# Kernel tuning notes

Hardware: AMD Instinct MI355X
Metric: run time of the kernel (lower is better)

The kernel has to match this reference:

```python
import math
import jax, jax.numpy as jnp
import numpy as np

COULOMB = 14.399645478425668  # eV*Angstrom / e^2


def setup_inputs() -> dict:
    key = jax.random.key(0)
    k0, k1, k2, k3, k4 = jax.random.split(key, 5)
    B, n, F, S = 128, 512, 64, 4  # molecules, atoms/molecule, feat dim, n species
    N = B * n
    node_features = jax.random.normal(k0, (N, F), dtype=jnp.float32)
    pos = jax.random.normal(k1, (N, 3), dtype=jnp.float32) * 5.0  # spread atoms out
    atom_type = jax.random.randint(k2, (N,), 0, S)
    total_charge = jnp.zeros((B, 1), dtype=jnp.float32)
    chi_weight = jax.random.normal(k3, (F, 1), dtype=jnp.float32) / np.float32(np.sqrt(F))
    hardness_param = jnp.ones((S,), dtype=jnp.float32)
    sigma = 0.3 + 0.5 * jax.random.uniform(k4, (S,), dtype=jnp.float32)  # covalent radii
    return dict(node_features=node_features, pos=pos, atom_type=atom_type,
                total_charge=total_charge, chi_weight=chi_weight,
                hardness_param=hardness_param, sigma=sigma, n_per_mol=n)


def reference(node_features, pos, atom_type, total_charge, chi_weight,
              hardness_param, sigma, n_per_mol):
    n = n_per_mol
    N, F = node_features.shape
    B = N // n

    feats = node_features.reshape(B, n, F)
    pos_b = pos.reshape(B, n, 3)
    sp = atom_type.reshape(B, n)

    chi = (feats @ chi_weight)[..., 0]                      # [B, n] electronegativity
    hard = jnp.square(hardness_param)[sp]                   # [B, n]
    sig = sigma[sp]                                         # [B, n]

    # pairwise distances within each molecule (diag masked for safe divide)
    diff = pos_b[:, :, None, :] - pos_b[:, None, :, :]      # [B, n, n, 3]
    d2 = jnp.sum(diff * diff, axis=-1)
    eye = jnp.eye(n, dtype=pos.dtype)
    d = jnp.sqrt(jnp.where(eye, 1.0, d2))                   # [B, n, n]

    gamma = jnp.sqrt(sig[:, :, None] ** 2 + sig[:, None, :] ** 2)
    off = COULOMB * jax.lax.erf(d / (math.sqrt(2.0) * gamma)) / d
    diag = hard + COULOMB / (math.sqrt(math.pi) * sig)      # [B, n]
    coeffs = off * (1.0 - eye) + eye * diag[:, :, None]     # [B, n, n]

    # augmented Qeq system with charge-conservation Lagrange multiplier
    A = jnp.ones((B, n + 1, n + 1), dtype=coeffs.dtype)
    A = A.at[:, :n, :n].set(coeffs)
    A = A.at[:, n, n].set(0.0)
    rhs = jnp.concatenate([-chi, total_charge], axis=1)     # [B, n+1]
    sol = jnp.linalg.solve(A, rhs[..., None])[..., 0]
    q = sol[:, :n]                                          # [B, n] charges

    # E = sum_{i<j} C_ij q_i q_j + sum_i (chi_i q_i + 0.5 diag_i q_i^2)
    #   = 0.5 q^T C q + chi . q   (C includes diagonal)
    e_qeq = 0.5 * jnp.einsum('bi,bij,bj->b', q, coeffs, q) + jnp.sum(chi * q, axis=1)
    return e_qeq[:, None], q.reshape(N, 1)
```

## Files before the change

kernel.cpp:

```cpp
#include <hip/hip_runtime.h>
#include <math.h>

#define NA 512
#define NN (NA*NA)
#define COULOMB 14.399645478425668f
#define SQRT_PI 1.7724538509055160273f

__device__ __forceinline__ float rl(float x, int lane) {
    return __int_as_float(__builtin_amdgcn_readlane(__float_as_int(x), lane));
}

__device__ __forceinline__ float pair_val(float dx, float dy, float dz,
                                          float s2i, float s2k) {
    float d2 = dx*dx + dy*dy + dz*dz;
    float rinv = rsqrtf(d2);
    return COULOMB * erff(d2 * rinv * rsqrtf(2.f * (s2i + s2k))) * rinv;
}

__global__ void k_pre(const float* __restrict__ feats, const float* __restrict__ w,
                      const int* __restrict__ type, const float* __restrict__ hard,
                      const float* __restrict__ sigma,
                      float* __restrict__ chi, float* __restrict__ diag,
                      float* __restrict__ sigA, int N) {
    __shared__ float wl[64];
    int tid = threadIdx.x;
    if (tid < 64) wl[tid] = w[tid];
    __syncthreads();
    int i = blockIdx.x * 256 + tid;
    if (i >= N) return;
    const float4* fp = (const float4*)(feats + (size_t)i * 64);
    float acc = 0.f;
#pragma unroll
    for (int q = 0; q < 16; q++) {
        float4 v = fp[q];
        acc += v.x * wl[4*q] + v.y * wl[4*q+1] + v.z * wl[4*q+2] + v.w * wl[4*q+3];
    }
    chi[i] = acc;
    int t = type[i];
    float s = sigma[t];
    float h = hard[t];
    sigA[i] = s;
    diag[i] = h * h + COULOMB / (SQRT_PI * s);
}

__global__ void __launch_bounds__(256, 1) k_panel(const float* __restrict__ pos,
                                                  const float* __restrict__ sigA,
                                                  const float* __restrict__ diagA,
                                                  float* __restrict__ C, const int j) {
    const int q = blockIdx.x;
    const int b = blockIdx.y;
    float* __restrict__ Cb = C + (size_t)b * NN;
    const int jb = j * 64;
    const int m = NA - jb - 64;
    const int tid = threadIdx.x;
    __shared__ float D[64 * 65];
    __shared__ float DT[64 * 64];
    __shared__ float invd[64];
    __shared__ float px[NA], py[NA], pz[NA], s2s[NA];

    if (j == 0) {
#pragma unroll
        for (int e = 0; e < 2; e++) {
            int i = e * 256 + tid;
            px[i] = pos[((size_t)b * NA + i) * 3 + 0];
            py[i] = pos[((size_t)b * NA + i) * 3 + 1];
            pz[i] = pos[((size_t)b * NA + i) * 3 + 2];
            float s = sigA[b * NA + i];
            s2s[i] = s * s;
        }
        __syncthreads();
    }

#pragma unroll
    for (int e = 0; e < 16; e++) {
        int f = e * 256 + tid;
        int rr = f >> 6, cc = f & 63;
        float v;
        if (j == 0) {
            if (rr == cc) v = diagA[b * NA + rr];
            else v = pair_val(px[rr]-px[cc], py[rr]-py[cc], pz[rr]-pz[cc], s2s[rr], s2s[cc]);
        } else {
            v = Cb[(size_t)(jb + rr) * NA + jb + cc];
        }
        D[rr * 65 + cc] = v;
    }

    const int h = m >> 1;
    const int r0 = q ? h : 0;
    const int nr = q ? (m - h) : h;
    const int r = tid - 32;
    const bool hasrow = (r >= 0 && r < nr);
    const int grow = jb + 64 + r0 + r;
    float rv[64];
    if (hasrow) {
        if (j == 0) {
#pragma unroll
            for (int k = 0; k < 64; k++)
                rv[k] = pair_val(px[grow]-px[k], py[grow]-py[k], pz[grow]-pz[k],
                                 s2s[grow], s2s[k]);
        } else {
            const float4* rp = (const float4*)(Cb + (size_t)grow * NA + jb);
#pragma unroll
            for (int qq = 0; qq < 16; qq++) {
                float4 v = rp[qq];
                rv[4*qq] = v.x; rv[4*qq+1] = v.y; rv[4*qq+2] = v.z; rv[4*qq+3] = v.w;
            }
        }
    }
    __syncthreads();

    if (tid < 64) {
        const int t = tid;
        float cl[64];
#pragma unroll
        for (int i = 0; i < 64; i++) cl[i] = (i >= t) ? D[i * 65 + t] : D[t * 65 + i];
#pragma unroll
        for (int k = 0; k < 64; k++) {
            float pivot = rl(cl[k], k);
            float invp = 1.0f / pivot;
            float factor = (t > k) ? (cl[k] * invp) : 0.0f;
#pragma unroll
            for (int i = k + 1; i < 64; i++) {
                float bc = rl(cl[i], k);
                cl[i] -= bc * factor;
            }
        }
        float rs = 1.0f / sqrtf(cl[t]);
        invd[t] = rs;
#pragma unroll
        for (int i = 0; i < 64; i++)
            if (i >= t) D[i * 65 + t] = cl[i] * rs;
    }
    __syncthreads();

#pragma unroll
    for (int e = 0; e < 16; e++) {
        int f = e * 256 + tid;
        int row = f >> 6, cc = f & 63;
        float v = D[row * 65 + cc];
        DT[row * 64 + cc] = (cc < row) ? v : 0.f;
        if (q == 0 && cc <= row) Cb[(size_t)(jb + row) * NA + jb + cc] = v;
    }
    __syncthreads();

    if (hasrow) {
#pragma unroll
        for (int k = 0; k < 64; k++) {
            float acc = rv[k];
            const float4* Lr = (const float4*)(DT + k * 64);
            const int k4 = k >> 2;
#pragma unroll
            for (int t4 = 0; t4 < k4; t4++) {
                float4 Lv = Lr[t4];
                acc -= Lv.x * rv[4*t4] + Lv.y * rv[4*t4+1] + Lv.z * rv[4*t4+2] + Lv.w * rv[4*t4+3];
            }
#pragma unroll
            for (int tt = k4 * 4; tt < k; tt++) acc -= DT[k * 64 + tt] * rv[tt];
            rv[k] = acc * invd[k];
        }
        float4* rp = (float4*)(Cb + (size_t)grow * NA + jb);
#pragma unroll
        for (int qq = 0; qq < 16; qq++)
            rp[qq] = make_float4(rv[4*qq], rv[4*qq+1], rv[4*qq+2], rv[4*qq+3]);
    }
}

template<bool GEN>
__global__ void __launch_bounds__(256, 3) k_trail(float* __restrict__ C,
                                                  const float* __restrict__ pos,
                                                  const float* __restrict__ sigA,
                                                  const float* __restrict__ diagA,
                                                  const int j) {
    const int b = blockIdx.y;
    float* __restrict__ Cb = C + (size_t)b * NN;
    const int jb = j * 64;
    const int m = NA - jb - 64;
    int t = blockIdx.x;
    int RI = 0;
    while (t >= RI + 1) { t -= RI + 1; RI++; }
    const int RJ = t;
    const int RB = RI * 128, CB = RJ * 128;
    const int vr = min(128, m - RB);
    const int vc = min(128, m - CB);
    const int tid = threadIdx.x;
    const int rg = tid >> 4, cg = tid & 15;

    __shared__ float As[128 * 65];
    __shared__ float Bs[128 * 65];

    float acc[8][8];

    if (GEN) {
        __shared__ float pAx[128], pAy[128], pAz[128], sA[128], dA[128];
        __shared__ float pBx[128], pBy[128], pBz[128], sB[128];
        if (tid < 128) {
            if (RB + tid < m) {
                int ga = b * NA + jb + 64 + RB + tid;
                pAx[tid] = pos[(size_t)ga * 3 + 0];
                pAy[tid] = pos[(size_t)ga * 3 + 1];
                pAz[tid] = pos[(size_t)ga * 3 + 2];
                float s = sigA[ga]; sA[tid] = s * s;
                dA[tid] = diagA[ga];
            }
        } else {
            int u = tid - 128;
            if (CB + u < m) {
                int gb = b * NA + jb + 64 + CB + u;
                pBx[u] = pos[(size_t)gb * 3 + 0];
                pBy[u] = pos[(size_t)gb * 3 + 1];
                pBz[u] = pos[(size_t)gb * 3 + 2];
                float s = sigA[gb]; sB[u] = s * s;
            }
        }
        __syncthreads();
#pragma unroll
        for (int rr = 0; rr < 8; rr++) {
            int row = rg * 8 + rr;
#pragma unroll
            for (int cc = 0; cc < 8; cc++) {
                int col = cg + 16 * cc;
                if (RB + row == CB + col)
                    acc[rr][cc] = dA[row];
                else
                    acc[rr][cc] = pair_val(pAx[row]-pBx[col], pAy[row]-pBy[col],
                                           pAz[row]-pBz[col], sA[row], sB[col]);
            }
        }
        __syncthreads();
    } else {
        const int GRB = jb + 64 + RB, GCB = jb + 64 + CB;
#pragma unroll
        for (int rr = 0; rr < 8; rr++) {
            int row = rg * 8 + rr;
#pragma unroll
            for (int cc = 0; cc < 8; cc++) {
                int col = cg + 16 * cc;
                acc[rr][cc] = (row < vr && col < vc)
                    ? Cb[(size_t)(GRB + row) * NA + GCB + col] : 0.f;
            }
        }
    }

    const float* Pan = Cb + (size_t)(jb + 64) * NA + jb;
#pragma unroll
    for (int e = 0; e < 8; e++) {
        int f = e * 256 + tid;
        int row = f >> 4, s = f & 15;
        float4 v = make_float4(0.f, 0.f, 0.f, 0.f);
        if (row < vr) v = *(const float4*)(Pan + (size_t)(RB + row) * NA + s * 4);
        As[row * 65 + s * 4 + 0] = v.x;
        As[row * 65 + s * 4 + 1] = v.y;
        As[row * 65 + s * 4 + 2] = v.z;
        As[row * 65 + s * 4 + 3] = v.w;
        float4 u = make_float4(0.f, 0.f, 0.f, 0.f);
        if (row < vc) u = *(const float4*)(Pan + (size_t)(CB + row) * NA + s * 4);
        Bs[row * 65 + s * 4 + 0] = u.x;
        Bs[row * 65 + s * 4 + 1] = u.y;
        Bs[row * 65 + s * 4 + 2] = u.z;
        Bs[row * 65 + s * 4 + 3] = u.w;
    }
    __syncthreads();

#pragma unroll 4
    for (int k = 0; k < 64; k++) {
        float ai[8], bj[8];
#pragma unroll
        for (int rr = 0; rr < 8; rr++) ai[rr] = As[(rg * 8 + rr) * 65 + k];
#pragma unroll
        for (int cc = 0; cc < 8; cc++) bj[cc] = Bs[(cg + 16 * cc) * 65 + k];
#pragma unroll
        for (int rr = 0; rr < 8; rr++)
#pragma unroll
            for (int cc = 0; cc < 8; cc++)
                acc[rr][cc] = fmaf(-ai[rr], bj[cc], acc[rr][cc]);
    }

    const int GRB = jb + 64 + RB, GCB = jb + 64 + CB;
#pragma unroll
    for (int rr = 0; rr < 8; rr++) {
        int row = rg * 8 + rr;
        if (row < vr) {
#pragma unroll
            for (int cc = 0; cc < 8; cc++) {
                int col = cg + 16 * cc;
                if (col < vc)
                    Cb[(size_t)(GRB + row) * NA + GCB + col] = acc[rr][cc];
            }
        }
    }
}

__global__ void __launch_bounds__(512, 1) k_tail(float* __restrict__ C) {
    const int b = blockIdx.x;
    float* __restrict__ Cb = C + (size_t)b * NN;
    const int base = NA - 192;
    const int tid = threadIdx.x;
    __shared__ float D[64 * 65];
    __shared__ float DT[64 * 64];
    __shared__ float invd[64];

    for (int t = 0; t < 3; t++) {
        const int jb = base + t * 64;
        const int mrem = 192 - t * 64 - 64;

#pragma unroll
        for (int e = 0; e < 8; e++) {
            int f = e * 512 + tid;
            int rr = f >> 6, cc = f & 63;
            D[rr * 65 + cc] = Cb[(size_t)(jb + rr) * NA + jb + cc];
        }
        __syncthreads();

        if (tid < 64) {
            const int tt = tid;
            float cl[64];
#pragma unroll
            for (int i = 0; i < 64; i++) cl[i] = (i >= tt) ? D[i * 65 + tt] : D[tt * 65 + i];
#pragma unroll
            for (int k = 0; k < 64; k++) {
                float pivot = rl(cl[k], k);
                float invp = 1.0f / pivot;
                float factor = (tt > k) ? (cl[k] * invp) : 0.0f;
#pragma unroll
                for (int i = k + 1; i < 64; i++) {
                    float bc = rl(cl[i], k);
                    cl[i] -= bc * factor;
                }
            }
            float rs = 1.0f / sqrtf(cl[tt]);
            invd[tt] = rs;
#pragma unroll
            for (int i = 0; i < 64; i++)
                if (i >= tt) D[i * 65 + tt] = cl[i] * rs;
        }
        __syncthreads();

#pragma unroll
        for (int e = 0; e < 8; e++) {
            int f = e * 512 + tid;
            int row = f >> 6, cc = f & 63;
            float v = D[row * 65 + cc];
            DT[row * 64 + cc] = (cc < row) ? v : 0.f;
            if (cc <= row) Cb[(size_t)(jb + row) * NA + jb + cc] = v;
        }
        __syncthreads();

        if (mrem == 0) break;

        const int r = tid - 64;
        if (r >= 0 && r < mrem) {
            const int grow = jb + 64 + r;
            float rv[64];
            const float4* rp = (const float4*)(Cb + (size_t)grow * NA + jb);
#pragma unroll
            for (int qq = 0; qq < 16; qq++) {
                float4 v = rp[qq];
                rv[4*qq] = v.x; rv[4*qq+1] = v.y; rv[4*qq+2] = v.z; rv[4*qq+3] = v.w;
            }
#pragma unroll
            for (int k = 0; k < 64; k++) {
                float acc = rv[k];
                const float4* Lr = (const float4*)(DT + k * 64);
                const int k4 = k >> 2;
#pragma unroll
                for (int t4 = 0; t4 < k4; t4++) {
                    float4 Lv = Lr[t4];
                    acc -= Lv.x * rv[4*t4] + Lv.y * rv[4*t4+1] + Lv.z * rv[4*t4+2] + Lv.w * rv[4*t4+3];
                }
#pragma unroll
                for (int ttt = k4 * 4; ttt < k; ttt++) acc -= DT[k * 64 + ttt] * rv[ttt];
                rv[k] = acc * invd[k];
            }
            float4* wp = (float4*)(Cb + (size_t)grow * NA + jb);
#pragma unroll
            for (int qq = 0; qq < 16; qq++)
                wp[qq] = make_float4(rv[4*qq], rv[4*qq+1], rv[4*qq+2], rv[4*qq+3]);
        }
        __threadfence_block();
        __syncthreads();

        if (mrem == 128) {
            const int rg = tid >> 5;
            const int cg = tid & 31;
            const int gr0 = jb + 64 + rg * 8;
            const int gc0 = jb + 64 + cg * 4;
            float acc[8][4];
#pragma unroll
            for (int rr = 0; rr < 8; rr++) {
                float4 v = *(const float4*)(Cb + (size_t)(gr0 + rr) * NA + gc0);
                acc[rr][0] = v.x; acc[rr][1] = v.y; acc[rr][2] = v.z; acc[rr][3] = v.w;
            }
#pragma unroll 4
            for (int k4 = 0; k4 < 16; k4++) {
                float4 a[8], bb[4];
#pragma unroll
                for (int rr = 0; rr < 8; rr++)
                    a[rr] = *(const float4*)(Cb + (size_t)(gr0 + rr) * NA + jb + k4 * 4);
#pragma unroll
                for (int cc = 0; cc < 4; cc++)
                    bb[cc] = *(const float4*)(Cb + (size_t)(gc0 + cc) * NA + jb + k4 * 4);
#pragma unroll
                for (int rr = 0; rr < 8; rr++) {
#pragma unroll
                    for (int cc = 0; cc < 4; cc++) {
                        acc[rr][cc] = fmaf(-a[rr].x, bb[cc].x, acc[rr][cc]);
                        acc[rr][cc] = fmaf(-a[rr].y, bb[cc].y, acc[rr][cc]);
                        acc[rr][cc] = fmaf(-a[rr].z, bb[cc].z, acc[rr][cc]);
                        acc[rr][cc] = fmaf(-a[rr].w, bb[cc].w, acc[rr][cc]);
                    }
                }
            }
#pragma unroll
            for (int rr = 0; rr < 8; rr++)
                *(float4*)(Cb + (size_t)(gr0 + rr) * NA + gc0) =
                    make_float4(acc[rr][0], acc[rr][1], acc[rr][2], acc[rr][3]);
        } else {
            const int rg = tid >> 6;
            const int col = tid & 63;
            const int gr0 = jb + 64 + rg * 8;
            const int gc = jb + 64 + col;
            float acc[8];
#pragma unroll
            for (int rr = 0; rr < 8; rr++)
                acc[rr] = Cb[(size_t)(gr0 + rr) * NA + gc];
#pragma unroll 4
            for (int k4 = 0; k4 < 16; k4++) {
                float4 bb = *(const float4*)(Cb + (size_t)gc * NA + jb + k4 * 4);
#pragma unroll
                for (int rr = 0; rr < 8; rr++) {
                    float4 a = *(const float4*)(Cb + (size_t)(gr0 + rr) * NA + jb + k4 * 4);
                    acc[rr] = fmaf(-a.x, bb.x, acc[rr]);
                    acc[rr] = fmaf(-a.y, bb.y, acc[rr]);
                    acc[rr] = fmaf(-a.z, bb.z, acc[rr]);
                    acc[rr] = fmaf(-a.w, bb.w, acc[rr]);
                }
            }
#pragma unroll
            for (int rr = 0; rr < 8; rr++)
                Cb[(size_t)(gr0 + rr) * NA + gc] = acc[rr];
        }
        __threadfence_block();
        __syncthreads();
    }
}

__global__ void __launch_bounds__(512, 1) k_solve(const float* __restrict__ C,
                                                  const float* __restrict__ chiA,
                                                  const float* __restrict__ Qtot,
                                                  float* __restrict__ out, int B) {
    int b = blockIdx.x;
    const float* Cb = C + (size_t)b * NN;
    int tid = threadIdx.x;
    __shared__ float D[64 * 65];
    __shared__ float r1[NA], r2[NA];
    __shared__ float pb1[4][NA], pb2[4][NA];
    __shared__ float red[16];
    __shared__ float muS;

    r1[tid] = chiA[b * NA + tid];
    r2[tid] = 1.0f;

    const int sub = tid & 7;
    const int rowg = tid >> 3;

    for (int j = 0; j < 8; j++) {
        const int jb = j * 64;
        __syncthreads();
#pragma unroll
        for (int e = 0; e < 8; e++) {
            int f = e * 512 + tid;
            int row = f >> 6, cc = f & 63;
            D[row * 65 + cc] = Cb[(size_t)(jb + row) * NA + jb + cc];
        }
        __syncthreads();
        if (tid < 128) {
            int lane = tid & 63;
            float* vv = (tid < 64) ? r1 : r2;
            float val = vv[jb + lane];
            float idg = 1.0f / D[lane * 65 + lane];
#pragma unroll
            for (int k = 0; k < 64; k++) {
                float yk = rl(val, k) * rl(idg, k);
                if (lane == k) vv[jb + k] = yk;
                float lv = (lane > k) ? D[lane * 65 + k] : 0.f;
                val -= lv * yk;
            }
        }
        __syncthreads();
#pragma unroll
        for (int p = 0; p < 7; p++) {
            int g = jb + 64 + p * 64 + rowg;
            if (g < NA) {
                const float4* Lr = (const float4*)(Cb + (size_t)g * NA + jb + sub * 8);
                float4 a0 = Lr[0], a1 = Lr[1];
                int y0 = jb + sub * 8;
                float d1 = a0.x*r1[y0]   + a0.y*r1[y0+1] + a0.z*r1[y0+2] + a0.w*r1[y0+3]
                         + a1.x*r1[y0+4] + a1.y*r1[y0+5] + a1.z*r1[y0+6] + a1.w*r1[y0+7];
                float d2 = a0.x*r2[y0]   + a0.y*r2[y0+1] + a0.z*r2[y0+2] + a0.w*r2[y0+3]
                         + a1.x*r2[y0+4] + a1.y*r2[y0+5] + a1.z*r2[y0+6] + a1.w*r2[y0+7];
                d1 += __shfl_xor(d1, 1); d2 += __shfl_xor(d2, 1);
                d1 += __shfl_xor(d1, 2); d2 += __shfl_xor(d2, 2);
                d1 += __shfl_xor(d1, 4); d2 += __shfl_xor(d2, 4);
                if (sub == 0) { r1[g] -= d1; r2[g] -= d2; }
            }
        }
    }

    const int ii = tid & 127;
    const int gg = tid >> 7;
    for (int j = 7; j >= 0; j--) {
        const int jb = j * 64;
        __syncthreads();
#pragma unroll
        for (int e = 0; e < 8; e++) {
            int f = e * 512 + tid;
            int row = f >> 6, cc = f & 63;
            D[row * 65 + cc] = Cb[(size_t)(jb + row) * NA + jb + cc];
        }
        __syncthreads();
        if (tid < 128) {
            int lane = tid & 63;
            float* vv = (tid < 64) ? r1 : r2;
            float val = vv[jb + lane];
            float idg = 1.0f / D[lane * 65 + lane];
#pragma unroll
            for (int k = 63; k >= 0; k--) {
                float xk = rl(val, k) * rl(idg, k);
                if (lane == k) vv[jb + k] = xk;
                float lv = (lane < k) ? D[k * 65 + lane] : 0.f;
                val -= lv * xk;
            }
        }
        __syncthreads();
        if (jb > 0) {
            const int nf4 = jb >> 2;
            float4 s1 = make_float4(0.f,0.f,0.f,0.f), s2 = make_float4(0.f,0.f,0.f,0.f);
            if (ii < nf4) {
#pragma unroll
                for (int gq = 0; gq < 16; gq++) {
                    int g = jb + gg * 16 + gq;
                    float x1 = r1[g], x2 = r2[g];
                    float4 Lv = *(const float4*)(Cb + (size_t)g * NA + ii * 4);
                    s1.x += Lv.x * x1; s1.y += Lv.y * x1; s1.z += Lv.z * x1; s1.w += Lv.w * x1;
                    s2.x += Lv.x * x2; s2.y += Lv.y * x2; s2.z += Lv.z * x2; s2.w += Lv.w * x2;
                }
            }
            *(float4*)(&pb1[gg][ii * 4]) = s1;
            *(float4*)(&pb2[gg][ii * 4]) = s2;
            __syncthreads();
            if (tid < jb) {
                r1[tid] -= pb1[0][tid] + pb1[1][tid] + pb1[2][tid] + pb1[3][tid];
                r2[tid] -= pb2[0][tid] + pb2[1][tid] + pb2[2][tid] + pb2[3][tid];
            }
        }
    }
    __syncthreads();

    float s1p = r1[tid], s2p = r2[tid];
#pragma unroll
    for (int off = 1; off < 64; off <<= 1) {
        s1p += __shfl_xor(s1p, off);
        s2p += __shfl_xor(s2p, off);
    }
    if ((tid & 63) == 0) { red[tid >> 6] = s1p; red[8 + (tid >> 6)] = s2p; }
    __syncthreads();
    if (tid == 0) {
        float s1 = 0.f, s2 = 0.f;
#pragma unroll
        for (int wv = 0; wv < 8; wv++) { s1 += red[wv]; s2 += red[8 + wv]; }
        muS = -(Qtot[b] + s1) / s2;
    }
    __syncthreads();
    float mu = muS;
    float qv = -r1[tid] - mu * r2[tid];
    out[B + (size_t)b * NA + tid] = qv;

    float eacc = chiA[b * NA + tid] * qv;
#pragma unroll
    for (int off = 1; off < 64; off <<= 1) eacc += __shfl_xor(eacc, off);
    __syncthreads();
    if ((tid & 63) == 0) red[tid >> 6] = eacc;
    __syncthreads();
    if (tid == 0) {
        float e = 0.f;
#pragma unroll
        for (int wv = 0; wv < 8; wv++) e += red[wv];
        out[b] = 0.5f * e - 0.5f * mu * Qtot[b];
    }
}

extern "C" void kernel_launch(void* const* d_in, const int* in_sizes, int n_in,
                              void* d_out, int out_size, void* d_ws, size_t ws_size,
                              hipStream_t stream) {
    const int B = in_sizes[3];
    const int N = in_sizes[2];
    const float* feats = (const float*)d_in[0];
    const float* pos   = (const float*)d_in[1];
    const int*   type  = (const int*)d_in[2];
    const float* Qt    = (const float*)d_in[3];
    const float* w     = (const float*)d_in[4];
    const float* hard  = (const float*)d_in[5];
    const float* sig   = (const float*)d_in[6];
    float* out = (float*)d_out;
    float* ws  = (float*)d_ws;

    float* C    = ws;
    float* chi  = ws + (size_t)B * NN;
    float* diag = chi + N;
    float* sigA = diag + N;

    k_pre<<<(N + 255) / 256, 256, 0, stream>>>(feats, w, type, hard, sig, chi, diag, sigA, N);

    static const int tilesJ[5] = {10, 6, 6, 3, 3};
    for (int j = 0; j < 5; j++) {
        k_panel<<<dim3(2, B), 256, 0, stream>>>(pos, sigA, diag, C, j);
        if (j == 0)
            k_trail<true><<<dim3(tilesJ[j], B), 256, 0, stream>>>(C, pos, sigA, diag, j);
        else
            k_trail<false><<<dim3(tilesJ[j], B), 256, 0, stream>>>(C, pos, sigA, diag, j);
    }
    k_tail<<<B, 512, 0, stream>>>(C);
    k_solve<<<B, 512, 0, stream>>>(C, chi, Qt, out, B);
}
```

Baseline: 767.1 us.

## Keep the 192x192 Cholesky tail block resident in LDS for all panel steps

The tail kernel now loads the whole trailing 192x192 block into a padded shared-memory tile once. It runs the three diagonal factorizations, the triangular solves and the trailing updates entirely in LDS, then writes the block back to global memory at the end. This removes the repeated global and L2 round-trips and the separate transposed diagonal copy used in each panel step. The cost is about 148 KB of LDS per block, which holds occupancy at one workgroup per CU. Shared-memory reads now replace the former float4 global loads in the inner loops.

Result: slower. 852.7 us (+11.2%).

```diff
diff --git a/kernel.cpp b/kernel.cpp
--- a/kernel.cpp
+++ b/kernel.cpp
@@ -290,32 +290,36 @@
     }
 }
 
+#define TS 193
 __global__ void __launch_bounds__(512, 1) k_tail(float* __restrict__ C) {
     const int b = blockIdx.x;
     float* __restrict__ Cb = C + (size_t)b * NN;
     const int base = NA - 192;
     const int tid = threadIdx.x;
-    __shared__ float D[64 * 65];
-    __shared__ float DT[64 * 64];
+    __shared__ float T[192 * TS];
     __shared__ float invd[64];
 
+    for (int f = tid; f < 192 * 48; f += 512) {
+        int lr = f / 48, lc4 = f % 48;
+        float4 v = *(const float4*)(Cb + (size_t)(base + lr) * NA + base + lc4 * 4);
+        T[lr * TS + lc4 * 4 + 0] = v.x;
+        T[lr * TS + lc4 * 4 + 1] = v.y;
+        T[lr * TS + lc4 * 4 + 2] = v.z;
+        T[lr * TS + lc4 * 4 + 3] = v.w;
+    }
+    __syncthreads();
+
     for (int t = 0; t < 3; t++) {
-        const int jb = base + t * 64;
-        const int mrem = 192 - t * 64 - 64;
-
-#pragma unroll
-        for (int e = 0; e < 8; e++) {
-            int f = e * 512 + tid;
-            int rr = f >> 6, cc = f & 63;
-            D[rr * 65 + cc] = Cb[(size_t)(jb + rr) * NA + jb + cc];
-        }
-        __syncthreads();
+        const int j0 = t * 64;
+        const int mrem = 128 - t * 64;
 
         if (tid < 64) {
             const int tt = tid;
             float cl[64];
 #pragma unroll
-            for (int i = 0; i < 64; i++) cl[i] = (i >= tt) ? D[i * 65 + tt] : D[tt * 65 + i];
+            for (int i = 0; i < 64; i++)
+                cl[i] = (i >= tt) ? T[(j0 + i) * TS + j0 + tt]
+                                  : T[(j0 + tt) * TS + j0 + i];
 #pragma unroll
             for (int k = 0; k < 64; k++) {
                 float pivot = rl(cl[k], k);
@@ -331,116 +335,83 @@
             invd[tt] = rs;
 #pragma unroll
             for (int i = 0; i < 64; i++)
-                if (i >= tt) D[i * 65 + tt] = cl[i] * rs;
-        }
-        __syncthreads();
-
-#pragma unroll
-        for (int e = 0; e < 8; e++) {
-            int f = e * 512 + tid;
-            int row = f >> 6, cc = f & 63;
-            float v = D[row * 65 + cc];
-            DT[row * 64 + cc] = (cc < row) ? v : 0.f;
-            if (cc <= row) Cb[(size_t)(jb + row) * NA + jb + cc] = v;
-        }
-        __syncthreads();
-
+                if (i >= tt) T[(j0 + i) * TS + j0 + tt] = cl[i] * rs;
+        }
+        __syncthreads();
         if (mrem == 0) break;
 
         const int r = tid - 64;
         if (r >= 0 && r < mrem) {
-            const int grow = jb + 64 + r;
+            const int lr = j0 + 64 + r;
             float rv[64];
-            const float4* rp = (const float4*)(Cb + (size_t)grow * NA + jb);
-#pragma unroll
-            for (int qq = 0; qq < 16; qq++) {
-                float4 v = rp[qq];
-                rv[4*qq] = v.x; rv[4*qq+1] = v.y; rv[4*qq+2] = v.z; rv[4*qq+3] = v.w;
-            }
+#pragma unroll
+            for (int k = 0; k < 64; k++) rv[k] = T[lr * TS + j0 + k];
 #pragma unroll
             for (int k = 0; k < 64; k++) {
                 float acc = rv[k];
-                const float4* Lr = (const float4*)(DT + k * 64);
-                const int k4 = k >> 2;
-#pragma unroll
-                for (int t4 = 0; t4 < k4; t4++) {
-                    float4 Lv = Lr[t4];
-                    acc -= Lv.x * rv[4*t4] + Lv.y * rv[4*t4+1] + Lv.z * rv[4*t4+2] + Lv.w * rv[4*t4+3];
-                }
-#pragma unroll
-                for (int ttt = k4 * 4; ttt < k; ttt++) acc -= DT[k * 64 + ttt] * rv[ttt];
+                const float* Lk = T + (j0 + k) * TS + j0;
+#pragma unroll 4
+                for (int tt = 0; tt < k; tt++) acc -= Lk[tt] * rv[tt];
                 rv[k] = acc * invd[k];
             }
-            float4* wp = (float4*)(Cb + (size_t)grow * NA + jb);
-#pragma unroll
-            for (int qq = 0; qq < 16; qq++)
-                wp[qq] = make_float4(rv[4*qq], rv[4*qq+1], rv[4*qq+2], rv[4*qq+3]);
-        }
-        __threadfence_block();
+#pragma unroll
+            for (int k = 0; k < 64; k++) T[lr * TS + j0 + k] = rv[k];
+        }
         __syncthreads();
 
         if (mrem == 128) {
-            const int rg = tid >> 5;
-            const int cg = tid & 31;
-            const int gr0 = jb + 64 + rg * 8;
-            const int gc0 = jb + 64 + cg * 4;
+            const int rg = tid >> 5, cg = tid & 31;
+            const int r0 = j0 + 64 + rg * 8, c0 = j0 + 64 + cg * 4;
             float acc[8][4];
 #pragma unroll
-            for (int rr = 0; rr < 8; rr++) {
-                float4 v = *(const float4*)(Cb + (size_t)(gr0 + rr) * NA + gc0);
-                acc[rr][0] = v.x; acc[rr][1] = v.y; acc[rr][2] = v.z; acc[rr][3] = v.w;
-            }
+            for (int rr = 0; rr < 8; rr++)
+#pragma unroll
+                for (int cc = 0; cc < 4; cc++)
+                    acc[rr][cc] = T[(r0 + rr) * TS + c0 + cc];
 #pragma unroll 4
-            for (int k4 = 0; k4 < 16; k4++) {
-                float4 a[8], bb[4];
+            for (int k = 0; k < 64; k++) {
+                float a[8], bb[4];
+#pragma unroll
+                for (int rr = 0; rr < 8; rr++) a[rr] = T[(r0 + rr) * TS + j0 + k];
+#pragma unroll
+                for (int cc = 0; cc < 4; cc++) bb[cc] = T[(c0 + cc) * TS + j0 + k];
 #pragma unroll
                 for (int rr = 0; rr < 8; rr++)
-                    a[rr] = *(const float4*)(Cb + (size_t)(gr0 + rr) * NA + jb + k4 * 4);
+#pragma unroll
+                    for (int cc = 0; cc < 4; cc++)
+                        acc[rr][cc] = fmaf(-a[rr], bb[cc], acc[rr][cc]);
+            }
+            __syncthreads();
+#pragma unroll
+            for (int rr = 0; rr < 8; rr++)
 #pragma unroll
                 for (int cc = 0; cc < 4; cc++)
-                    bb[cc] = *(const float4*)(Cb + (size_t)(gc0 + cc) * NA + jb + k4 * 4);
-#pragma unroll
-                for (int rr = 0; rr < 8; rr++) {
-#pragma unroll
-                    for (int cc = 0; cc < 4; cc++) {
-                        acc[rr][cc] = fmaf(-a[rr].x, bb[cc].x, acc[rr][cc]);
-                        acc[rr][cc] = fmaf(-a[rr].y, bb[cc].y, acc[rr][cc]);
-                        acc[rr][cc] = fmaf(-a[rr].z, bb[cc].z, acc[rr][cc]);
-                        acc[rr][cc] = fmaf(-a[rr].w, bb[cc].w, acc[rr][cc]);
-                    }
-                }
-            }
-#pragma unroll
-            for (int rr = 0; rr < 8; rr++)
-                *(float4*)(Cb + (size_t)(gr0 + rr) * NA + gc0) =
-                    make_float4(acc[rr][0], acc[rr][1], acc[rr][2], acc[rr][3]);
+                    T[(r0 + rr) * TS + c0 + cc] = acc[rr][cc];
         } else {
-            const int rg = tid >> 6;
-            const int col = tid & 63;
-            const int gr0 = jb + 64 + rg * 8;
-            const int gc = jb + 64 + col;
+            const int rg = tid >> 6, col = tid & 63;
+            const int r0 = j0 + 64 + rg * 8, c = j0 + 64 + col;
             float acc[8];
 #pragma unroll
-            for (int rr = 0; rr < 8; rr++)
-                acc[rr] = Cb[(size_t)(gr0 + rr) * NA + gc];
+            for (int rr = 0; rr < 8; rr++) acc[rr] = T[(r0 + rr) * TS + c];
 #pragma unroll 4
-            for (int k4 = 0; k4 < 16; k4++) {
-                float4 bb = *(const float4*)(Cb + (size_t)gc * NA + jb + k4 * 4);
-#pragma unroll
-                for (int rr = 0; rr < 8; rr++) {
-                    float4 a = *(const float4*)(Cb + (size_t)(gr0 + rr) * NA + jb + k4 * 4);
-                    acc[rr] = fmaf(-a.x, bb.x, acc[rr]);
-                    acc[rr] = fmaf(-a.y, bb.y, acc[rr]);
-                    acc[rr] = fmaf(-a.z, bb.z, acc[rr]);
-                    acc[rr] = fmaf(-a.w, bb.w, acc[rr]);
-                }
-            }
-#pragma unroll
-            for (int rr = 0; rr < 8; rr++)
-                Cb[(size_t)(gr0 + rr) * NA + gc] = acc[rr];
-        }
-        __threadfence_block();
-        __syncthreads();
+            for (int k = 0; k < 64; k++) {
+                float bv = T[c * TS + j0 + k];
+#pragma unroll
+                for (int rr = 0; rr < 8; rr++)
+                    acc[rr] = fmaf(-T[(r0 + rr) * TS + j0 + k], bv, acc[rr]);
+            }
+            __syncthreads();
+#pragma unroll
+            for (int rr = 0; rr < 8; rr++) T[(r0 + rr) * TS + c] = acc[rr];
+        }
+        __syncthreads();
+    }
+
+    for (int f = tid; f < 192 * 48; f += 512) {
+        int lr = f / 48, lc4 = f % 48;
+        float4 v = make_float4(T[lr * TS + lc4 * 4 + 0], T[lr * TS + lc4 * 4 + 1],
+                               T[lr * TS + lc4 * 4 + 2], T[lr * TS + lc4 * 4 + 3]);
+        *(float4*)(Cb + (size_t)(base + lr) * NA + base + lc4 * 4) = v;
     }
 }
 
```
